# Performance work log

Hardware: AMD Instinct MI355X
Metric: run time of the kernel (lower is better)

Reference implementation:

```python
import jax, jax.numpy as jnp
import numpy as np

N_ACT = 3  # [relu, tanh, sigmoid]


def setup_inputs() -> dict:
    key = jax.random.key(0)
    k1, k2, k3 = jax.random.split(key, 3)
    B, IN, OUT = 4096, 4096, 4096
    x = jax.random.normal(k1, (B, IN), dtype=jnp.float32)
    W = jax.random.normal(k2, (OUT, IN), dtype=jnp.float32)
    b = jax.random.normal(k3, (OUT,), dtype=jnp.float32)
    return {"x": x, "W": W, "b": b}


def reference(x, W, b):
    # Linear: y = x @ W^T + b  -> [B, OUT]
    y = jnp.einsum("bi,oi->bo", x, W) + b
    # Per-output-column criterion: mean over batch, then idx = int(mean % 3).
    # torch `%` on tensors is remainder with the divisor's sign (non-negative
    # here), and int() then truncates == floor for non-negative values.
    means = jnp.mean(y, axis=0)                        # [OUT]
    idx = jnp.mod(means, float(N_ACT)).astype(jnp.int32)  # [OUT] in {0,1,2}
    idx_b = idx[None, :]                               # broadcast over batch
    # Device-side branchless select among the three activations.
    out = jnp.where(
        idx_b == 0,
        jax.nn.relu(y),
        jnp.where(idx_b == 1, jnp.tanh(y), jax.nn.sigmoid(y)),
    )
    return out
```

## Files before the change

kernel.cpp:

```cpp
#include <hip/hip_runtime.h>
#include <hip/hip_bf16.h>
#include <math.h>

#define B_DIM   4096
#define IN_DIM  4096
#define OUT_DIM 4096

typedef __attribute__((ext_vector_type(8))) short  short8;
typedef __attribute__((ext_vector_type(4))) float  floatx4;

__device__ __forceinline__ ushort f2bf(float f) {
    unsigned b = __float_as_uint(f);
    return (ushort)((b + 0x7fffu + ((b >> 16) & 1u)) >> 16);
}

__global__ void cvt_x_colsum(const float* __restrict__ x, ushort* __restrict__ xb,
                             double* __restrict__ part) {
    int c0 = blockIdx.x * 1024 + threadIdx.x * 4;
    int r0 = blockIdx.y * 16;
    double s0 = 0, s1 = 0, s2 = 0, s3 = 0;
#pragma unroll 4
    for (int r = 0; r < 16; ++r) {
        size_t off = (size_t)(r0 + r) * IN_DIM + c0;
        float4 v = *(const float4*)(x + off);
        ushort4 o;
        o.x = f2bf(v.x); o.y = f2bf(v.y); o.z = f2bf(v.z); o.w = f2bf(v.w);
        *(ushort4*)(xb + off) = o;
        s0 += (double)v.x; s1 += (double)v.y; s2 += (double)v.z; s3 += (double)v.w;
    }
    double* p = part + (size_t)blockIdx.y * IN_DIM + c0;
    p[0] = s0; p[1] = s1; p[2] = s2; p[3] = s3;
}

__global__ void xbar_reduce(const double* __restrict__ part, double* __restrict__ xbar) {
    __shared__ double red[256];
    int col   = blockIdx.x * 64 + (threadIdx.x & 63);
    int slice = threadIdx.x >> 6;
    double s = 0.0;
    for (int rb = slice * 64; rb < slice * 64 + 64; ++rb)
        s += part[(size_t)rb * IN_DIM + col];
    red[threadIdx.x] = s;
    __syncthreads();
    if (slice == 0) {
        double v = red[threadIdx.x] + red[threadIdx.x + 64]
                 + red[threadIdx.x + 128] + red[threadIdx.x + 192];
        xbar[col] = v * (1.0 / (double)B_DIM);
    }
}

__global__ void cvt_w_means(const float* __restrict__ W, const float* __restrict__ bias,
                            const double* __restrict__ xbar, ushort* __restrict__ wb,
                            int* __restrict__ idx) {
    __shared__ double red[256];
    int o = blockIdx.x;
    size_t base = (size_t)o * IN_DIM;
    double s = 0.0;
#pragma unroll
    for (int j = 0; j < 4; ++j) {
        int i = j * 1024 + threadIdx.x * 4;
        float4 v = *(const float4*)(W + base + i);
        ushort4 ob;
        ob.x = f2bf(v.x); ob.y = f2bf(v.y); ob.z = f2bf(v.z); ob.w = f2bf(v.w);
        *(ushort4*)(wb + base + i) = ob;
        double2 xv0 = *(const double2*)(xbar + i);
        double2 xv1 = *(const double2*)(xbar + i + 2);
        s += (double)v.x * xv0.x + (double)v.y * xv0.y
           + (double)v.z * xv1.x + (double)v.w * xv1.y;
    }
    red[threadIdx.x] = s;
    __syncthreads();
    for (int st = 128; st > 0; st >>= 1) {
        if (threadIdx.x < st) red[threadIdx.x] += red[threadIdx.x + st];
        __syncthreads();
    }
    if (threadIdx.x == 0) {
        float mf = (float)(red[0] + (double)bias[o]);
        float md = fmodf(mf, 3.0f);
        if (md < 0.0f) md += 3.0f;
        idx[o] = (int)md;
    }
}

__global__ void __launch_bounds__(256) gemm_bt_act(
    const ushort* __restrict__ A,
    const ushort* __restrict__ Bt,
    const float*  __restrict__ bias,
    const int*    __restrict__ idx,
    float*        __restrict__ out) {
    __shared__ __align__(16) ushort As[128 * 64];
    __shared__ __align__(16) ushort Bs[128 * 64];

    const int t    = threadIdx.x;
    const int w    = t >> 6;
    const int l    = t & 63;
    const int quad = l >> 4;
    const int lrow = l & 15;

    const int b   = blockIdx.y * 32 + blockIdx.x;
    const int sup = b >> 6;
    const int q   = b & 63;
    const int m0  = ((sup >> 2) * 8 + (q >> 3)) * 128;
    const int n0  = ((sup & 3)  * 8 + (q & 7))  * 128;

    const int m0w  = (w >> 1) * 64;
    const int n0w  = (w & 1) * 64;
    const int K    = IN_DIM;

    floatx4 acc[4][4] = {};

    for (int k0 = 0; k0 < K; k0 += 64) {
#pragma unroll
        for (int j = 0; j < 4; ++j) {
            int chunk = j * 256 + t;
            int r     = chunk >> 3;
            int kb    = (chunk & 7) ^ (r & 7);
            int goff  = kb << 3;
            int ldsoff = (j * 256 + w * 64) * 8;
            __builtin_amdgcn_global_load_lds(
                (__attribute__((address_space(1))) void*)(A + (size_t)(m0 + r) * K + k0 + goff),
                (__attribute__((address_space(3))) void*)(As + ldsoff), 16, 0, 0);
            __builtin_amdgcn_global_load_lds(
                (__attribute__((address_space(1))) void*)(Bt + (size_t)(n0 + r) * K + k0 + goff),
                (__attribute__((address_space(3))) void*)(Bs + ldsoff), 16, 0, 0);
        }
        __syncthreads();

#pragma unroll
        for (int s = 0; s < 2; ++s) {
            short8 af[4], bf[4];
#pragma unroll
            for (int mi = 0; mi < 4; ++mi) {
                int r = m0w + mi * 16 + lrow;
                int kb = (s * 4 + quad) ^ (r & 7);
                af[mi] = *(const short8*)&As[r * 64 + kb * 8];
            }
#pragma unroll
            for (int ni = 0; ni < 4; ++ni) {
                int r = n0w + ni * 16 + lrow;
                int kb = (s * 4 + quad) ^ (r & 7);
                bf[ni] = *(const short8*)&Bs[r * 64 + kb * 8];
            }
#pragma unroll
            for (int mi = 0; mi < 4; ++mi)
#pragma unroll
                for (int ni = 0; ni < 4; ++ni)
                    acc[mi][ni] = __builtin_amdgcn_mfma_f32_16x16x32_bf16(
                        af[mi], bf[ni], acc[mi][ni], 0, 0, 0);
        }
        __syncthreads();
    }

#pragma unroll
    for (int ni = 0; ni < 4; ++ni) {
        int   col     = n0 + n0w + ni * 16 + lrow;
        int   id      = idx[col];
        float bv      = bias[col];
        float a       = (id == 1) ? -2.0f : -1.0f;
        bool  isrelu  = (id == 0);
        bool  istanh  = (id == 1);
#pragma unroll
        for (int mi = 0; mi < 4; ++mi) {
            int rowb = m0 + m0w + mi * 16 + quad * 4;
#pragma unroll
            for (int r = 0; r < 4; ++r) {
                float y   = acc[mi][ni][r] + bv;
                float e   = __expf(a * y);
                float s   = __builtin_amdgcn_rcpf(1.0f + e);
                float act = istanh ? fmaf(2.0f, s, -1.0f) : s;
                float v   = isrelu ? fmaxf(y, 0.0f) : act;
                out[(size_t)(rowb + r) * OUT_DIM + col] = v;
            }
        }
    }
}

extern "C" void kernel_launch(void* const* d_in, const int* in_sizes, int n_in,
                              void* d_out, int out_size, void* d_ws, size_t ws_size,
                              hipStream_t stream) {
    const float* x = (const float*)d_in[0];
    const float* W = (const float*)d_in[1];
    const float* b = (const float*)d_in[2];
    float* out = (float*)d_out;

    char* ws = (char*)d_ws;
    ushort* xb   = (ushort*)(ws);
    ushort* wb   = (ushort*)(ws + (33554432));
    double* part = (double*)(ws + (67108864));
    double* xbar = (double*)(ws + (67108864 + 8388608));
    int*    idx  = (int*)   (ws + (67108864 + 8388608 + 32768));

    cvt_x_colsum<<<dim3(4, 256), 256, 0, stream>>>(x, xb, part);
    xbar_reduce<<<64, 256, 0, stream>>>(part, xbar);
    cvt_w_means<<<4096, 256, 0, stream>>>(W, b, xbar, wb, idx);
    gemm_bt_act<<<dim3(32, 32), 256, 0, stream>>>(xb, wb, b, idx, out);
}
```

Before: 344.4 us.

## Merge x and W bf16 conversion into one prep kernel, reorder GEMM tiles

Converts W to bf16 alongside x in a single prep kernel, so the means kernel only reads W and no longer writes wb. This gives the prep launch more parallel work, but W is now read twice from memory, once in prep and once in the means kernel. The GEMM drops the grouped tile swizzle in favour of a plain row-major block mapping, which may cost L2 reuse. It also loads bias and idx before the K loop and raises wave priority with s_setprio around the MFMA section.

```diff
diff --git a/kernel.cpp b/kernel.cpp
--- a/kernel.cpp
+++ b/kernel.cpp
@@ -14,22 +14,36 @@
     return (ushort)((b + 0x7fffu + ((b >> 16) & 1u)) >> 16);
 }
 
-__global__ void cvt_x_colsum(const float* __restrict__ x, ushort* __restrict__ xb,
-                             double* __restrict__ part) {
-    int c0 = blockIdx.x * 1024 + threadIdx.x * 4;
-    int r0 = blockIdx.y * 16;
-    double s0 = 0, s1 = 0, s2 = 0, s3 = 0;
+__global__ void prep(const float* __restrict__ x, const float* __restrict__ W,
+                     ushort* __restrict__ xb, ushort* __restrict__ wb,
+                     double* __restrict__ part) {
+    int bid = blockIdx.x;
+    if (bid < 1024) {
+        int c0 = (bid & 3) * 1024 + threadIdx.x * 4;
+        int r0 = (bid >> 2) * 16;
+        double s0 = 0, s1 = 0, s2 = 0, s3 = 0;
 #pragma unroll 4
-    for (int r = 0; r < 16; ++r) {
-        size_t off = (size_t)(r0 + r) * IN_DIM + c0;
-        float4 v = *(const float4*)(x + off);
-        ushort4 o;
-        o.x = f2bf(v.x); o.y = f2bf(v.y); o.z = f2bf(v.z); o.w = f2bf(v.w);
-        *(ushort4*)(xb + off) = o;
-        s0 += (double)v.x; s1 += (double)v.y; s2 += (double)v.z; s3 += (double)v.w;
-    }
-    double* p = part + (size_t)blockIdx.y * IN_DIM + c0;
-    p[0] = s0; p[1] = s1; p[2] = s2; p[3] = s3;
+        for (int r = 0; r < 16; ++r) {
+            size_t off = (size_t)(r0 + r) * IN_DIM + c0;
+            float4 v = *(const float4*)(x + off);
+            ushort4 o;
+            o.x = f2bf(v.x); o.y = f2bf(v.y); o.z = f2bf(v.z); o.w = f2bf(v.w);
+            *(ushort4*)(xb + off) = o;
+            s0 += (double)v.x; s1 += (double)v.y; s2 += (double)v.z; s3 += (double)v.w;
+        }
+        double* p = part + (size_t)(bid >> 2) * IN_DIM + c0;
+        p[0] = s0; p[1] = s1; p[2] = s2; p[3] = s3;
+    } else {
+        const size_t total = (size_t)OUT_DIM * IN_DIM;
+        size_t i = ((size_t)(bid - 1024) * 256 + threadIdx.x) * 4;
+        const size_t stride = (size_t)1024 * 256 * 4;
+        for (; i < total; i += stride) {
+            float4 v = *(const float4*)(W + i);
+            ushort4 o;
+            o.x = f2bf(v.x); o.y = f2bf(v.y); o.z = f2bf(v.z); o.w = f2bf(v.w);
+            *(ushort4*)(wb + i) = o;
+        }
+    }
 }
 
 __global__ void xbar_reduce(const double* __restrict__ part, double* __restrict__ xbar) {
@@ -48,9 +62,8 @@
     }
 }
 
-__global__ void cvt_w_means(const float* __restrict__ W, const float* __restrict__ bias,
-                            const double* __restrict__ xbar, ushort* __restrict__ wb,
-                            int* __restrict__ idx) {
+__global__ void means_idx(const float* __restrict__ W, const float* __restrict__ bias,
+                          const double* __restrict__ xbar, int* __restrict__ idx) {
     __shared__ double red[256];
     int o = blockIdx.x;
     size_t base = (size_t)o * IN_DIM;
@@ -59,9 +72,6 @@
     for (int j = 0; j < 4; ++j) {
         int i = j * 1024 + threadIdx.x * 4;
         float4 v = *(const float4*)(W + base + i);
-        ushort4 ob;
-        ob.x = f2bf(v.x); ob.y = f2bf(v.y); ob.z = f2bf(v.z); ob.w = f2bf(v.w);
-        *(ushort4*)(wb + base + i) = ob;
         double2 xv0 = *(const double2*)(xbar + i);
         double2 xv1 = *(const double2*)(xbar + i + 2);
         s += (double)v.x * xv0.x + (double)v.y * xv0.y
@@ -95,16 +105,20 @@
     const int l    = t & 63;
     const int quad = l >> 4;
     const int lrow = l & 15;
-
-    const int b   = blockIdx.y * 32 + blockIdx.x;
-    const int sup = b >> 6;
-    const int q   = b & 63;
-    const int m0  = ((sup >> 2) * 8 + (q >> 3)) * 128;
-    const int n0  = ((sup & 3)  * 8 + (q & 7))  * 128;
-
+    const int m0   = blockIdx.y * 128;
+    const int n0   = blockIdx.x * 128;
     const int m0w  = (w >> 1) * 64;
     const int n0w  = (w & 1) * 64;
     const int K    = IN_DIM;
+
+    int   idv[4];
+    float bvv[4];
+#pragma unroll
+    for (int ni = 0; ni < 4; ++ni) {
+        int col = n0 + n0w + ni * 16 + lrow;
+        idv[ni] = idx[col];
+        bvv[ni] = bias[col];
+    }
 
     floatx4 acc[4][4] = {};
 
@@ -125,6 +139,7 @@
         }
         __syncthreads();
 
+        asm volatile("s_setprio 1");
 #pragma unroll
         for (int s = 0; s < 2; ++s) {
             short8 af[4], bf[4];
@@ -147,14 +162,15 @@
                     acc[mi][ni] = __builtin_amdgcn_mfma_f32_16x16x32_bf16(
                         af[mi], bf[ni], acc[mi][ni], 0, 0, 0);
         }
+        asm volatile("s_setprio 0");
         __syncthreads();
     }
 
 #pragma unroll
     for (int ni = 0; ni < 4; ++ni) {
         int   col     = n0 + n0w + ni * 16 + lrow;
-        int   id      = idx[col];
-        float bv      = bias[col];
+        int   id      = idv[ni];
+        float bv      = bvv[ni];
         float a       = (id == 1) ? -2.0f : -1.0f;
         bool  isrelu  = (id == 0);
         bool  istanh  = (id == 1);
@@ -189,8 +205,8 @@
     double* xbar = (double*)(ws + (67108864 + 8388608));
     int*    idx  = (int*)   (ws + (67108864 + 8388608 + 32768));
 
-    cvt_x_colsum<<<dim3(4, 256), 256, 0, stream>>>(x, xb, part);
+    prep<<<2048, 256, 0, stream>>>(x, W, xb, wb, part);
     xbar_reduce<<<64, 256, 0, stream>>>(part, xbar);
-    cvt_w_means<<<4096, 256, 0, stream>>>(W, b, xbar, wb, idx);
+    means_idx<<<4096, 256, 0, stream>>>(W, b, xbar, idx);
     gemm_bt_act<<<dim3(32, 32), 256, 0, stream>>>(xb, wb, b, idx, out);
 }
```

After: 364.6 us. 5.8% more time.

## Double-buffer GEMM LDS tiles with K=32 stages to overlap loads and MFMA

Applied to the files above, without the earlier changes.

Splits the K=64 single-buffered LDS tile into two K=32 ping-pong buffers, so the global-to-LDS loads for the next stage are issued before computing on the current stage. This aims to hide global load latency behind MFMA work. It also drops the XOR swizzle: with 64-byte rows, the ds_read pattern may now hit LDS bank conflicts. The K-step per sync halves, which adds barrier overhead.

```diff
diff --git a/kernel.cpp b/kernel.cpp
--- a/kernel.cpp
+++ b/kernel.cpp
@@ -81,14 +81,48 @@
     }
 }
 
+#define STAGE(AS, BS, KS)                                                          \
+    _Pragma("unroll")                                                              \
+    for (int j = 0; j < 2; ++j) {                                                  \
+        int chunk = j * 256 + t;                                                   \
+        int r     = chunk >> 2;                                                    \
+        int kc    = (chunk & 3) << 3;                                              \
+        int ldsoff = (j * 256 + w * 64) * 8;                                       \
+        __builtin_amdgcn_global_load_lds(                                          \
+            (__attribute__((address_space(1))) void*)(A + (size_t)(m0 + r) * K + (KS) * 32 + kc),  \
+            (__attribute__((address_space(3))) void*)(AS + ldsoff), 16, 0, 0);     \
+        __builtin_amdgcn_global_load_lds(                                          \
+            (__attribute__((address_space(1))) void*)(Bt + (size_t)(n0 + r) * K + (KS) * 32 + kc), \
+            (__attribute__((address_space(3))) void*)(BS + ldsoff), 16, 0, 0);     \
+    }
+
+#define COMPUTE(AS, BS)                                                            \
+    {                                                                              \
+        short8 af[4], bf[4];                                                       \
+        _Pragma("unroll")                                                          \
+        for (int mi = 0; mi < 4; ++mi)                                             \
+            af[mi] = *(const short8*)&AS[(m0w + mi * 16 + lrow) * 32 + quad * 8];  \
+        _Pragma("unroll")                                                          \
+        for (int ni = 0; ni < 4; ++ni)                                             \
+            bf[ni] = *(const short8*)&BS[(n0w + ni * 16 + lrow) * 32 + quad * 8];  \
+        _Pragma("unroll")                                                          \
+        for (int mi = 0; mi < 4; ++mi)                                             \
+            _Pragma("unroll")                                                      \
+            for (int ni = 0; ni < 4; ++ni)                                         \
+                acc[mi][ni] = __builtin_amdgcn_mfma_f32_16x16x32_bf16(             \
+                    af[mi], bf[ni], acc[mi][ni], 0, 0, 0);                         \
+    }
+
 __global__ void __launch_bounds__(256) gemm_bt_act(
     const ushort* __restrict__ A,
     const ushort* __restrict__ Bt,
     const float*  __restrict__ bias,
     const int*    __restrict__ idx,
     float*        __restrict__ out) {
-    __shared__ __align__(16) ushort As[128 * 64];
-    __shared__ __align__(16) ushort Bs[128 * 64];
+    __shared__ __align__(16) ushort As0[128 * 32];
+    __shared__ __align__(16) ushort Bs0[128 * 32];
+    __shared__ __align__(16) ushort As1[128 * 32];
+    __shared__ __align__(16) ushort Bs1[128 * 32];
 
     const int t    = threadIdx.x;
     const int w    = t >> 6;
@@ -108,46 +142,14 @@
 
     floatx4 acc[4][4] = {};
 
-    for (int k0 = 0; k0 < K; k0 += 64) {
-#pragma unroll
-        for (int j = 0; j < 4; ++j) {
-            int chunk = j * 256 + t;
-            int r     = chunk >> 3;
-            int kb    = (chunk & 7) ^ (r & 7);
-            int goff  = kb << 3;
-            int ldsoff = (j * 256 + w * 64) * 8;
-            __builtin_amdgcn_global_load_lds(
-                (__attribute__((address_space(1))) void*)(A + (size_t)(m0 + r) * K + k0 + goff),
-                (__attribute__((address_space(3))) void*)(As + ldsoff), 16, 0, 0);
-            __builtin_amdgcn_global_load_lds(
-                (__attribute__((address_space(1))) void*)(Bt + (size_t)(n0 + r) * K + k0 + goff),
-                (__attribute__((address_space(3))) void*)(Bs + ldsoff), 16, 0, 0);
-        }
+    STAGE(As0, Bs0, 0)
+    for (int ks = 0; ks < 128; ks += 2) {
         __syncthreads();
-
-#pragma unroll
-        for (int s = 0; s < 2; ++s) {
-            short8 af[4], bf[4];
-#pragma unroll
-            for (int mi = 0; mi < 4; ++mi) {
-                int r = m0w + mi * 16 + lrow;
-                int kb = (s * 4 + quad) ^ (r & 7);
-                af[mi] = *(const short8*)&As[r * 64 + kb * 8];
-            }
-#pragma unroll
-            for (int ni = 0; ni < 4; ++ni) {
-                int r = n0w + ni * 16 + lrow;
-                int kb = (s * 4 + quad) ^ (r & 7);
-                bf[ni] = *(const short8*)&Bs[r * 64 + kb * 8];
-            }
-#pragma unroll
-            for (int mi = 0; mi < 4; ++mi)
-#pragma unroll
-                for (int ni = 0; ni < 4; ++ni)
-                    acc[mi][ni] = __builtin_amdgcn_mfma_f32_16x16x32_bf16(
-                        af[mi], bf[ni], acc[mi][ni], 0, 0, 0);
-        }
+        STAGE(As1, Bs1, ks + 1)
+        COMPUTE(As0, Bs0)
         __syncthreads();
+        if (ks + 2 < 128) STAGE(As0, Bs0, ks + 2)
+        COMPUTE(As1, Bs1)
     }
 
 #pragma unroll
```

Result: slower. 360.8 us (+4.7%).
